# Optimization experiments

Hardware: AMD Instinct MI355X
Metric: run time of the kernel (lower is better)

Reference implementation:

```python
import jax, jax.numpy as jnp
import numpy as np

G = 160          # voxel grid extent per axis
N = 300000       # active voxels
CIN, COUT = 64, 128
EPS = 1e-4       # BatchNorm eps from module (0.0001)


def _neighbor_table(pos):
    """pos: [N,3] int32 in [0,G). Returns idx [27,N] int32, -1 where no neighbor voxel exists."""
    n = pos.shape[0]
    flat = (pos[:, 0] * G + pos[:, 1]) * G + pos[:, 2]
    grid = jnp.full((G * G * G,), -1, dtype=jnp.int32).at[flat].set(
        jnp.arange(n, dtype=jnp.int32))
    offs = jnp.array([[dx, dy, dz] for dx in (-1, 0, 1)
                      for dy in (-1, 0, 1) for dz in (-1, 0, 1)], dtype=jnp.int32)
    npos = pos[None, :, :] + offs[:, None, :]              # [27,N,3]
    inb = jnp.all((npos >= 0) & (npos < G), axis=-1)       # [27,N]
    nflat = (npos[..., 0] * G + npos[..., 1]) * G + npos[..., 2]
    nflat = jnp.where(inb, nflat, 0)
    return jnp.where(inb, grid[nflat], -1)                 # [27,N]


def _sparse_conv(feat, nbr_idx, W):
    """Submanifold sparse 3x3x3 conv. feat [N,Cin], nbr_idx [27,N], W [27,Cin,Cout]."""
    n = feat.shape[0]
    acc0 = jnp.zeros((n, W.shape[-1]), dtype=feat.dtype)

    def body(acc, xs):
        idx, Wk = xs                                       # [N], [Cin,Cout]
        valid = (idx >= 0)
        g = feat[jnp.maximum(idx, 0)] * valid[:, None].astype(feat.dtype)
        return acc + g @ Wk, None

    out, _ = jax.lax.scan(body, acc0, (nbr_idx, W))
    return out


def _bn(x, gamma, beta, mean, var):
    # eval-mode BatchNorm1d: (x - mean) / sqrt(var + eps) * gamma + beta
    return (x - mean) * jax.lax.rsqrt(var + EPS) * gamma + beta


def setup_inputs() -> dict:
    key = jax.random.key(0)
    ks = jax.random.split(key, 8)
    rng = np.random.default_rng(0)
    flat = rng.choice(G * G * G, size=N, replace=False)
    pos = np.stack(np.unravel_index(flat, (G, G, G)), axis=-1).astype(np.int32)

    feat = jax.random.normal(ks[0], (N, CIN), dtype=jnp.float32)
    lin_w = jax.random.normal(ks[1], (COUT, CIN), dtype=jnp.float32) / np.sqrt(CIN)
    W1 = jax.random.normal(ks[2], (27, CIN, COUT), dtype=jnp.float32) / np.sqrt(27 * CIN)
    W2 = jax.random.normal(ks[3], (27, COUT, COUT), dtype=jnp.float32) / np.sqrt(27 * COUT)
    return {
        "feat": feat,
        "pos": jnp.asarray(pos),
        "lin_w": lin_w,
        "bn1_gamma": jnp.ones((CIN,), jnp.float32),
        "bn1_beta": jnp.zeros((CIN,), jnp.float32),
        "bn1_mean": 0.1 * jax.random.normal(ks[4], (CIN,), dtype=jnp.float32),
        "bn1_var": 0.5 + jax.random.uniform(ks[5], (CIN,), dtype=jnp.float32),
        "W1": W1,
        "bn2_gamma": jnp.ones((COUT,), jnp.float32),
        "bn2_beta": jnp.zeros((COUT,), jnp.float32),
        "bn2_mean": 0.1 * jax.random.normal(ks[6], (COUT,), dtype=jnp.float32),
        "bn2_var": 0.5 + jax.random.uniform(ks[7], (COUT,), dtype=jnp.float32),
        "W2": W2,
    }


def reference(feat, pos, lin_w, bn1_gamma, bn1_beta, bn1_mean, bn1_var, W1,
              bn2_gamma, bn2_beta, bn2_mean, bn2_var, W2):
    nbr_idx = _neighbor_table(pos)                     # [27,N]
    out1 = feat @ lin_w.T                              # NetworkInNetwork skip
    h = jnp.maximum(_bn(feat, bn1_gamma, bn1_beta, bn1_mean, bn1_var), 0.0)  # LeakyReLU(0)==ReLU
    h = _sparse_conv(h, nbr_idx, W1)
    h = jnp.maximum(_bn(h, bn2_gamma, bn2_beta, bn2_mean, bn2_var), 0.0)
    h = _sparse_conv(h, nbr_idx, W2)
    return out1 + h
```

## Files before the change

kernel.cpp:

```cpp
#include <hip/hip_runtime.h>

#define G    160
#define G3   (G*G*G)
#define NV   300000
#define EPS  1e-4f
#define CAP  24576
#define CPAD 32
#define PCAP 655360
#define TOTIDX 896

typedef unsigned short u16;
typedef __attribute__((ext_vector_type(8))) short bf16x8;
typedef __attribute__((ext_vector_type(4))) float f32x4;

#define OFF_PART 0ull
#define OFF_GRID 0ull
#define OFF_PIN  167772160ull
#define OFF_PDST (OFF_PIN  + 2654208ull)
#define OFF_RI   (OFF_PDST + 2654208ull)
#define OFF_CNT  (OFF_RI   + 1200000ull)
#define OFF_H0   (OFF_CNT  + 4096ull)
#define OFF_H1   (OFF_H0   + 38400000ull)
#define OFF_W1T  (OFF_H1   + 76800000ull)
#define OFF_W2T  (OFF_W1T  + 442368ull)
#define OFF_LINW (OFF_W2T  + 884736ull)
#define OFF_BNP  (OFF_LINW + 16384ull)
#define WS_NEED  (OFF_BNP  + 1024ull)

__device__ __forceinline__ u16 f2bf(float f) {
  unsigned u = __float_as_uint(f);
  return (u16)((u + 0x7fffu + ((u >> 16) & 1u)) >> 16);
}
__device__ __forceinline__ float bf2f(u16 h) {
  return __uint_as_float(((unsigned)h) << 16);
}

__global__ void k_grid(const int* __restrict__ pos, int* __restrict__ grid) {
  int i = blockIdx.x * 256 + threadIdx.x;
  if (i < NV)
    grid[(pos[3*i] * G + pos[3*i+1]) * G + pos[3*i+2]] = i;
}

__global__ __launch_bounds__(256) void k_pairs(const int* __restrict__ pos,
                        const int* __restrict__ grid,
                        int* __restrict__ pin, int* __restrict__ pdst,
                        int* __restrict__ rowinfo, int* __restrict__ counts) {
  __shared__ int lcnt[27];
  __shared__ int wboff[27][4];
  __shared__ int gbase[27];
  __shared__ int scan[256];
  __shared__ int sgb;
  int t = threadIdx.x, lane = t & 63, wv = t >> 6;
  if (t < 27) lcnt[t] = 0;
  int i = blockIdx.x * 256 + t;
  bool act = (i < NV);
  int p0 = 0, p1 = 1 << 20, p2 = 0;
  if (act) { p0 = pos[3*i]; p1 = pos[3*i+1]; p2 = pos[3*i+2]; }
  __syncthreads();

  int j[26];
  #pragma unroll
  for (int kk = 0; kk < 26; kk++) {
    int k = kk < 13 ? kk : kk + 1;
    int q0 = p0 + k/9 - 1, q1 = p1 + (k/3)%3 - 1, q2 = p2 + k%3 - 1;
    bool inb = (q0 >= 0 && q0 < G && q1 >= 0 && q1 < G && q2 >= 0 && q2 < G);
    int addr = inb ? (q0*G + q1)*G + q2 : 0;
    int jj = grid[addr];
    j[kk] = inb ? jj : -1;
  }

  unsigned vmask = 0;
  #pragma unroll
  for (int kk = 0; kk < 26; kk++) if (j[kk] >= 0) vmask |= 1u << kk;
  int ci = __popc(vmask);

  unsigned long long m[26];
  #pragma unroll
  for (int kk = 0; kk < 26; kk++) m[kk] = __ballot(j[kk] >= 0);

  #pragma unroll
  for (int kk = 0; kk < 26; kk++) {
    int k = kk < 13 ? kk : kk + 1;
    if (lane == 0) wboff[k][wv] = atomicAdd(&lcnt[k], (int)__popcll(m[kk]));
  }
  scan[t] = ci;
  __syncthreads();
  #pragma unroll
  for (int d = 1; d < 256; d <<= 1) {
    int val = (t >= d) ? scan[t - d] : 0;
    __syncthreads();
    scan[t] += val;
    __syncthreads();
  }
  if (t < 27 && t != 13)
    gbase[t] = atomicAdd(&counts[t * CPAD], lcnt[t]);
  if (t == 255) sgb = atomicAdd(&counts[TOTIDX], scan[255]);
  __syncthreads();

  int rbase = sgb + scan[t] - ci;
  int cw = (rbase + ci > PCAP) ? 0 : ci;
  if (act) rowinfo[i] = (rbase << 5) | cw;

  #pragma unroll
  for (int kk = 0; kk < 26; kk++) {
    if (j[kk] >= 0) {
      int k = kk < 13 ? kk : kk + 1;
      int slot = gbase[k] + wboff[k][wv] + (int)__popcll(m[kk] & ((1ull << lane) - 1ull));
      int dst = rbase + __popc(vmask & ((1u << kk) - 1u));
      if (slot < CAP) {
        pin[k*CAP + slot]  = j[kk];
        pdst[k*CAP + slot] = (dst < PCAP) ? dst : -1;
      }
    }
  }
}

__global__ void k_bn1(const float* __restrict__ feat, const float* g, const float* b,
                      const float* m, const float* v, u16* __restrict__ h0) {
  __shared__ float ss[64], tt[64];
  int t = threadIdx.x;
  if (t < 64) { float s = g[t] * rsqrtf(v[t] + EPS); ss[t] = s; tt[t] = b[t] - m[t]*s; }
  __syncthreads();
  long gt = (long)blockIdx.x * 256 + t;
  if (gt >= (long)NV * 16) return;
  int c = (int)(gt & 15) * 4;
  float4 x = ((const float4*)feat)[gt];
  ushort4 q;
  q.x = f2bf(fmaxf(x.x*ss[c  ] + tt[c  ], 0.f));
  q.y = f2bf(fmaxf(x.y*ss[c+1] + tt[c+1], 0.f));
  q.z = f2bf(fmaxf(x.z*ss[c+2] + tt[c+2], 0.f));
  q.w = f2bf(fmaxf(x.w*ss[c+3] + tt[c+3], 0.f));
  ((ushort4*)h0)[gt] = q;
}

__global__ void k_weights(const float* __restrict__ W1, const float* __restrict__ W2,
                          const float* __restrict__ linw,
                          const float* __restrict__ g2, const float* __restrict__ b2,
                          const float* __restrict__ m2, const float* __restrict__ v2,
                          u16* __restrict__ w1t, u16* __restrict__ w2t, u16* __restrict__ lwt,
                          float* __restrict__ bnp) {
  __shared__ float tmp[8192];
  int b = blockIdx.x, t = threadIdx.x;
  if (b < 27) {
    const float* src = W1 + b * 8192;
    u16* dst = w1t + b * 8192;
    for (int u = t; u < 8192; u += 256) tmp[u] = src[u];
    __syncthreads();
    for (int u = t; u < 8192; u += 256) { int c = u >> 6, a = u & 63; dst[c*64 + a] = f2bf(tmp[a*128 + c]); }
  } else if (b < 54) {
    int k = b - 27;
    const float* src = W2 + k * 16384;
    u16* dst = w2t + k * 16384;
    for (int h = 0; h < 2; h++) {
      for (int u = t; u < 8192; u += 256) tmp[u] = src[h*8192 + u];
      __syncthreads();
      for (int u = t; u < 8192; u += 256) { int c = u >> 6, a = u & 63; dst[c*128 + h*64 + a] = f2bf(tmp[a*128 + c]); }
      __syncthreads();
    }
  } else if (b == 54) {
    for (int u = t; u < 8192; u += 256) lwt[u] = f2bf(linw[u]);
  } else {
    if (t < 128) { float s = g2[t] * rsqrtf(v2[t] + EPS); bnp[t] = s; bnp[128 + t] = b2[t] - m2[t]*s; }
  }
}

template<int K, int RS>
__device__ __forceinline__ void stage_rows(const u16* __restrict__ src, const int* sidx, u16* lds) {
  const int LPR = K / 8, RPI = 256 / LPR;
  int t = threadIdx.x, o = t % LPR, r0 = t / LPR;
  #pragma unroll
  for (int r = r0; r < 128; r += RPI) {
    int j = sidx[r];
    int4 val = make_int4(0, 0, 0, 0);
    if (j >= 0) val = *(const int4*)(src + (long)j * RS + o * 8);
    *(int4*)(lds + r * (K + 8) + o * 8) = val;
  }
}

__device__ __forceinline__ void stage_feat(const float* __restrict__ feat, int row0, u16* lds) {
  int t = threadIdx.x, o = t & 15, r0 = t >> 4;
  #pragma unroll
  for (int r = r0; r < 128; r += 16) {
    int row = row0 + r;
    float4 x = make_float4(0.f, 0.f, 0.f, 0.f);
    if (row < NV) x = *(const float4*)(feat + (long)row * 64 + o * 4);
    ushort4 q; q.x = f2bf(x.x); q.y = f2bf(x.y); q.z = f2bf(x.z); q.w = f2bf(x.w);
    *(ushort4*)(lds + r * 72 + o * 4) = q;
  }
}

template<int K>
__device__ __forceinline__ void mma_tile(const u16* As, const u16* __restrict__ wt, f32x4 acc[4][4]) {
  int lane = threadIdx.x & 63, wave = threadIdx.x >> 6;
  int wr = (wave >> 1) * 64, wc = (wave & 1) * 64;
  int lr = lane & 15, lk = (lane >> 4) * 8;
  #pragma unroll
  for (int kk = 0; kk < K; kk += 32) {
    bf16x8 a[4], b[4];
    #pragma unroll
    for (int f = 0; f < 4; f++) a[f] = *(const bf16x8*)(As + (wr + f*16 + lr) * (K + 8) + kk + lk);
    #pragma unroll
    for (int f = 0; f < 4; f++) b[f] = *(const bf16x8*)(wt + (wc + f*16 + lr) * K + kk + lk);
    #pragma unroll
    for (int fr = 0; fr < 4; fr++)
      #pragma unroll
      for (int fc = 0; fc < 4; fc++)
        acc[fr][fc] = __builtin_amdgcn_mfma_f32_16x16x32_bf16(a[fr], b[fc], acc[fr][fc], 0, 0, 0);
  }
}

__device__ __forceinline__ void spill_acc(const f32x4 acc[4][4], u16* As) {
  int t = threadIdx.x, lane = t & 63, wave = t >> 6;
  int wr = (wave >> 1) * 64, wc = (wave & 1) * 64, cr = (lane >> 4) * 4, cc = lane & 15;
  #pragma unroll
  for (int fr = 0; fr < 4; fr++)
    #pragma unroll
    for (int r = 0; r < 4; r++)
      #pragma unroll
      for (int fc = 0; fc < 4; fc++)
        As[(wr + fr*16 + cr + r) * 136 + wc + fc*16 + cc] = f2bf(acc[fr][fc][r]);
}

template<int K, int RS>
__global__ __launch_bounds__(256, 4) void k_scat(const u16* __restrict__ h, const u16* __restrict__ wt,
                                                 const int* __restrict__ pin,
                                                 const int* __restrict__ pdst,
                                                 const int* __restrict__ counts,
                                                 u16* __restrict__ partial) {
  int k = blockIdx.y;
  int cnt = counts[k * CPAD]; if (cnt > CAP) cnt = CAP;
  int base = blockIdx.x * 128;
  if (base >= cnt) return;
  __shared__ __align__(16) u16 As[128 * 136];
  __shared__ int sin[128], sdst[128];
  int t = threadIdx.x;
  if (t < 128) sin[t] = (base + t < cnt) ? pin[k*CAP + base + t] : -1;
  else         sdst[t - 128] = (base + t - 128 < cnt) ? pdst[k*CAP + base + t - 128] : -1;
  __syncthreads();
  stage_rows<K, RS>(h, sin, As);
  __syncthreads();
  f32x4 acc[4][4] = {};
  mma_tile<K>(As, wt + k * (K * 128), acc);
  __syncthreads();
  spill_acc(acc, As);
  __syncthreads();
  #pragma unroll
  for (int u = t; u < 2048; u += 256) {
    int r = u >> 4, o = u & 15;
    int d = sdst[r];
    if (d >= 0)
      *(int4*)(partial + (long)d * 128 + o * 8) = *(const int4*)(As + r * 136 + o * 8);
  }
}

__global__ __launch_bounds__(256, 4) void k_self1(const u16* __restrict__ h0,
                                                  const u16* __restrict__ w1t,
                                                  u16* __restrict__ h1) {
  __shared__ __align__(16) u16 As[128 * 136];
  __shared__ int sidx[128];
  int t = threadIdx.x, row0 = blockIdx.x * 128;
  if (t < 128) sidx[t] = (row0 + t < NV) ? row0 + t : -1;
  __syncthreads();
  stage_rows<64, 64>(h0, sidx, As);
  __syncthreads();
  f32x4 acc[4][4] = {};
  mma_tile<64>(As, w1t + 13 * 8192, acc);
  __syncthreads();
  spill_acc(acc, As);
  __syncthreads();
  #pragma unroll
  for (int u = t; u < 2048; u += 256) {
    int r = u >> 4, o = u & 15;
    if (row0 + r < NV)
      *(int4*)(h1 + (long)(row0 + r) * 128 + o * 8) = *(const int4*)(As + r * 136 + o * 8);
  }
}

__global__ __launch_bounds__(256, 4) void k_self2(const float* __restrict__ feat,
                                                  const u16* __restrict__ lwt,
                                                  u16* __restrict__ h1,
                                                  const u16* __restrict__ w2t) {
  __shared__ __align__(16) u16 As[128 * 136];
  __shared__ int sidx[128];
  int t = threadIdx.x, row0 = blockIdx.x * 128;
  if (t < 128) sidx[t] = (row0 + t < NV) ? row0 + t : -1;
  __syncthreads();
  f32x4 acc[4][4] = {};
  stage_feat(feat, row0, As);
  __syncthreads();
  mma_tile<64>(As, lwt, acc);
  __syncthreads();
  stage_rows<128, 128>(h1, sidx, As);
  __syncthreads();
  mma_tile<128>(As, w2t + 13 * 16384, acc);
  __syncthreads();
  spill_acc(acc, As);
  __syncthreads();
  #pragma unroll
  for (int u = t; u < 2048; u += 256) {
    int r = u >> 4, o = u & 15;
    if (row0 + r < NV)
      *(int4*)(h1 + (long)(row0 + r) * 128 + o * 8) = *(const int4*)(As + r * 136 + o * 8);
  }
}

__device__ __forceinline__ void gather_csr(int row, int q, int base, int cnt,
                                           const u16* __restrict__ sp,
                                           const u16* __restrict__ partial,
                                           float c[32]) {
  bf16x8 s0[4];
  const u16* srow = sp + (long)row * 128 + q * 32;
  #pragma unroll
  for (int u = 0; u < 4; u++) s0[u] = *(const bf16x8*)(srow + u * 8);
  #pragma unroll
  for (int u = 0; u < 4; u++)
    #pragma unroll
    for (int e = 0; e < 8; e++) c[u*8 + e] = bf2f((u16)s0[u][e]);
  const u16* pr = partial + (long)base * 128 + q * 32;
  int p = 0;
  for (; p + 2 <= cnt; p += 2) {
    bf16x8 a[4], b[4];
    #pragma unroll
    for (int u = 0; u < 4; u++) a[u] = *(const bf16x8*)(pr + u * 8);
    #pragma unroll
    for (int u = 0; u < 4; u++) b[u] = *(const bf16x8*)(pr + 128 + u * 8);
    #pragma unroll
    for (int u = 0; u < 4; u++)
      #pragma unroll
      for (int e = 0; e < 8; e++) c[u*8 + e] += bf2f((u16)a[u][e]) + bf2f((u16)b[u][e]);
    pr += 256;
  }
  if (p < cnt) {
    bf16x8 a[4];
    #pragma unroll
    for (int u = 0; u < 4; u++) a[u] = *(const bf16x8*)(pr + u * 8);
    #pragma unroll
    for (int u = 0; u < 4; u++)
      #pragma unroll
      for (int e = 0; e < 8; e++) c[u*8 + e] += bf2f((u16)a[u][e]);
  }
}

__global__ __launch_bounds__(256) void k_gather1(const int* __restrict__ rowinfo,
                                                 const u16* __restrict__ partial,
                                                 const float* __restrict__ bnp,
                                                 u16* __restrict__ h1) {
  long tid = (long)blockIdx.x * 256 + threadIdx.x;
  int row = (int)(tid >> 2), q = (int)(tid & 3);
  if (row >= NV) return;
  int ri = rowinfo[row];
  int base = (int)((unsigned)ri >> 5), cnt = ri & 31;
  float c[32];
  gather_csr(row, q, base, cnt, h1, partial, c);
  int col0 = q * 32;
  unsigned w[16];
  #pragma unroll
  for (int e = 0; e < 16; e++) {
    float o0 = fmaxf(c[2*e  ] * bnp[col0 + 2*e  ] + bnp[128 + col0 + 2*e  ], 0.f);
    float o1 = fmaxf(c[2*e+1] * bnp[col0 + 2*e+1] + bnp[128 + col0 + 2*e+1], 0.f);
    w[e] = (unsigned)f2bf(o0) | ((unsigned)f2bf(o1) << 16);
  }
  int4* dst = (int4*)(h1 + (long)row * 128 + col0);
  #pragma unroll
  for (int u = 0; u < 4; u++) dst[u] = make_int4(w[4*u], w[4*u+1], w[4*u+2], w[4*u+3]);
}

__global__ __launch_bounds__(256) void k_gather2(const int* __restrict__ rowinfo,
                                                 const u16* __restrict__ partial,
                                                 const u16* __restrict__ h1,
                                                 float* __restrict__ out) {
  long tid = (long)blockIdx.x * 256 + threadIdx.x;
  int row = (int)(tid >> 2), q = (int)(tid & 3);
  if (row >= NV) return;
  int ri = rowinfo[row];
  int base = (int)((unsigned)ri >> 5), cnt = ri & 31;
  float c[32];
  gather_csr(row, q, base, cnt, h1, partial, c);
  float* dst = out + (long)row * 128 + q * 32;
  #pragma unroll
  for (int u = 0; u < 8; u++) {
    f32x4 v;
    #pragma unroll
    for (int e = 0; e < 4; e++) v[e] = c[u*4 + e];
    *(f32x4*)(dst + u * 4) = v;
  }
}

extern "C" void kernel_launch(void* const* d_in, const int* in_sizes, int n_in,
                              void* d_out, int out_size, void* d_ws, size_t ws_size,
                              hipStream_t stream) {
  const float* feat = (const float*)d_in[0];
  const int*   pos  = (const int*)d_in[1];
  const float* linw = (const float*)d_in[2];
  const float* g1 = (const float*)d_in[3], *b1 = (const float*)d_in[4];
  const float* m1 = (const float*)d_in[5], *v1 = (const float*)d_in[6];
  const float* W1 = (const float*)d_in[7];
  const float* g2 = (const float*)d_in[8], *b2 = (const float*)d_in[9];
  const float* m2 = (const float*)d_in[10], *v2 = (const float*)d_in[11];
  const float* W2 = (const float*)d_in[12];

  if (ws_size < WS_NEED) return;

  char* ws = (char*)d_ws;
  u16*   partial = (u16*)(ws + OFF_PART);
  int*   grid    = (int*)(ws + OFF_GRID);
  int*   pin     = (int*)(ws + OFF_PIN);
  int*   pdst    = (int*)(ws + OFF_PDST);
  int*   rowinfo = (int*)(ws + OFF_RI);
  int*   counts  = (int*)(ws + OFF_CNT);
  u16*   h0      = (u16*)(ws + OFF_H0);
  u16*   h1      = (u16*)(ws + OFF_H1);
  u16*   w1t     = (u16*)(ws + OFF_W1T);
  u16*   w2t     = (u16*)(ws + OFF_W2T);
  u16*   lwt     = (u16*)(ws + OFF_LINW);
  float* bnp     = (float*)(ws + OFF_BNP);
  float* out     = (float*)d_out;

  hipMemsetAsync(grid,  0xFF, (size_t)G3 * 4, stream);
  hipMemsetAsync(counts, 0, 4096, stream);

  k_grid  <<<(NV + 255) / 256, 256, 0, stream>>>(pos, grid);
  k_pairs <<<(NV + 255) / 256, 256, 0, stream>>>(pos, grid, pin, pdst, rowinfo, counts);
  k_bn1   <<<(NV * 16) / 256, 256, 0, stream>>>(feat, g1, b1, m1, v1, h0);
  k_weights<<<56, 256, 0, stream>>>(W1, W2, linw, g2, b2, m2, v2, w1t, w2t, lwt, bnp);

  dim3 gt((NV + 127) / 128);
  dim3 gscat(CAP / 128, 27);
  dim3 gg(((long)NV * 4 + 255) / 256);
  k_scat<64, 64>   <<<gscat, 256, 0, stream>>>(h0, w1t, pin, pdst, counts, partial);
  k_self1          <<<gt, 256, 0, stream>>>(h0, w1t, h1);
  k_gather1        <<<gg, 256, 0, stream>>>(rowinfo, partial, bnp, h1);
  k_scat<128, 128> <<<gscat, 256, 0, stream>>>(h1, w2t, pin, pdst, counts, partial);
  k_self2          <<<gt, 256, 0, stream>>>(feat, lwt, h1, w2t);
  k_gather2        <<<gg, 256, 0, stream>>>(rowinfo, partial, h1, out);
}
```

Measured before the change: 676.8 us.

## Halve GEMM tile rows to 64 and fuse scatter with self conv1

Cuts the per-block row tile from 128 to 64 in the scatter and self-GEMM kernels. This halves the accumulator registers and LDS per block and raises the launch-bounds occupancy hint from 4 to 6. The first scatter and self kernels are merged into a single launch with a flat block index, which removes one launch and lets the two kinds of work overlap. The trade-off is twice as many blocks, with less weight reuse per block and more index and sync overhead.

```diff
diff --git a/kernel.cpp b/kernel.cpp
--- a/kernel.cpp
+++ b/kernel.cpp
@@ -8,6 +8,7 @@
 #define CPAD 32
 #define PCAP 655360
 #define TOTIDX 896
+#define NSCAT (27*384)
 
 typedef unsigned short u16;
 typedef __attribute__((ext_vector_type(8))) short bf16x8;
@@ -169,7 +170,7 @@
   const int LPR = K / 8, RPI = 256 / LPR;
   int t = threadIdx.x, o = t % LPR, r0 = t / LPR;
   #pragma unroll
-  for (int r = r0; r < 128; r += RPI) {
+  for (int r = r0; r < 64; r += RPI) {
     int j = sidx[r];
     int4 val = make_int4(0, 0, 0, 0);
     if (j >= 0) val = *(const int4*)(src + (long)j * RS + o * 8);
@@ -180,7 +181,7 @@
 __device__ __forceinline__ void stage_feat(const float* __restrict__ feat, int row0, u16* lds) {
   int t = threadIdx.x, o = t & 15, r0 = t >> 4;
   #pragma unroll
-  for (int r = r0; r < 128; r += 16) {
+  for (int r = r0; r < 64; r += 16) {
     int row = row0 + r;
     float4 x = make_float4(0.f, 0.f, 0.f, 0.f);
     if (row < NV) x = *(const float4*)(feat + (long)row * 64 + o * 4);
@@ -190,30 +191,30 @@
 }
 
 template<int K>
-__device__ __forceinline__ void mma_tile(const u16* As, const u16* __restrict__ wt, f32x4 acc[4][4]) {
+__device__ __forceinline__ void mma_tile(const u16* As, const u16* __restrict__ wt, f32x4 acc[2][4]) {
   int lane = threadIdx.x & 63, wave = threadIdx.x >> 6;
-  int wr = (wave >> 1) * 64, wc = (wave & 1) * 64;
+  int wr = (wave >> 1) * 32, wc = (wave & 1) * 64;
   int lr = lane & 15, lk = (lane >> 4) * 8;
   #pragma unroll
   for (int kk = 0; kk < K; kk += 32) {
-    bf16x8 a[4], b[4];
-    #pragma unroll
-    for (int f = 0; f < 4; f++) a[f] = *(const bf16x8*)(As + (wr + f*16 + lr) * (K + 8) + kk + lk);
+    bf16x8 a[2], b[4];
+    #pragma unroll
+    for (int f = 0; f < 2; f++) a[f] = *(const bf16x8*)(As + (wr + f*16 + lr) * (K + 8) + kk + lk);
     #pragma unroll
     for (int f = 0; f < 4; f++) b[f] = *(const bf16x8*)(wt + (wc + f*16 + lr) * K + kk + lk);
     #pragma unroll
-    for (int fr = 0; fr < 4; fr++)
+    for (int fr = 0; fr < 2; fr++)
       #pragma unroll
       for (int fc = 0; fc < 4; fc++)
         acc[fr][fc] = __builtin_amdgcn_mfma_f32_16x16x32_bf16(a[fr], b[fc], acc[fr][fc], 0, 0, 0);
   }
 }
 
-__device__ __forceinline__ void spill_acc(const f32x4 acc[4][4], u16* As) {
+__device__ __forceinline__ void spill_acc(const f32x4 acc[2][4], u16* As) {
   int t = threadIdx.x, lane = t & 63, wave = t >> 6;
-  int wr = (wave >> 1) * 64, wc = (wave & 1) * 64, cr = (lane >> 4) * 4, cc = lane & 15;
-  #pragma unroll
-  for (int fr = 0; fr < 4; fr++)
+  int wr = (wave >> 1) * 32, wc = (wave & 1) * 64, cr = (lane >> 4) * 4, cc = lane & 15;
+  #pragma unroll
+  for (int fr = 0; fr < 2; fr++)
     #pragma unroll
     for (int r = 0; r < 4; r++)
       #pragma unroll
@@ -221,31 +222,82 @@
         As[(wr + fr*16 + cr + r) * 136 + wc + fc*16 + cc] = f2bf(acc[fr][fc][r]);
 }
 
-template<int K, int RS>
-__global__ __launch_bounds__(256, 4) void k_scat(const u16* __restrict__ h, const u16* __restrict__ wt,
-                                                 const int* __restrict__ pin,
-                                                 const int* __restrict__ pdst,
-                                                 const int* __restrict__ counts,
-                                                 u16* __restrict__ partial) {
+__global__ __launch_bounds__(256, 6) void k_c1(const u16* __restrict__ h0,
+                                               const u16* __restrict__ w1t,
+                                               const int* __restrict__ pin,
+                                               const int* __restrict__ pdst,
+                                               const int* __restrict__ counts,
+                                               u16* __restrict__ partial,
+                                               u16* __restrict__ h1) {
+  __shared__ __align__(16) u16 As[64 * 136];
+  __shared__ int sin[64], sdst[64];
+  int bx = blockIdx.x, t = threadIdx.x;
+  if (bx < NSCAT) {
+    int k = bx / 384, base = (bx % 384) * 64;
+    int cnt = counts[k * CPAD]; if (cnt > CAP) cnt = CAP;
+    if (base >= cnt) return;
+    if (t < 64)       sin[t]       = (base + t < cnt)      ? pin[k*CAP + base + t]       : -1;
+    else if (t < 128) sdst[t - 64] = (base + t - 64 < cnt) ? pdst[k*CAP + base + t - 64] : -1;
+    __syncthreads();
+    stage_rows<64, 64>(h0, sin, As);
+    __syncthreads();
+    f32x4 acc[2][4] = {};
+    mma_tile<64>(As, w1t + k * 8192, acc);
+    __syncthreads();
+    spill_acc(acc, As);
+    __syncthreads();
+    #pragma unroll
+    for (int u = t; u < 1024; u += 256) {
+      int r = u >> 4, o = u & 15;
+      int d = sdst[r];
+      if (d >= 0)
+        *(int4*)(partial + (long)d * 128 + o * 8) = *(const int4*)(As + r * 136 + o * 8);
+    }
+  } else {
+    int row0 = (bx - NSCAT) * 64;
+    if (t < 64) sin[t] = (row0 + t < NV) ? row0 + t : -1;
+    __syncthreads();
+    stage_rows<64, 64>(h0, sin, As);
+    __syncthreads();
+    f32x4 acc[2][4] = {};
+    mma_tile<64>(As, w1t + 13 * 8192, acc);
+    __syncthreads();
+    spill_acc(acc, As);
+    __syncthreads();
+    #pragma unroll
+    for (int u = t; u < 1024; u += 256) {
+      int r = u >> 4, o = u & 15;
+      if (row0 + r < NV)
+        *(int4*)(h1 + (long)(row0 + r) * 128 + o * 8) = *(const int4*)(As + r * 136 + o * 8);
+    }
+  }
+}
+
+__global__ __launch_bounds__(256, 6) void k_scat2(const u16* __restrict__ h1,
+                                                  const u16* __restrict__ w2t,
+                                                  const int* __restrict__ pin,
+                                                  const int* __restrict__ pdst,
+                                                  const int* __restrict__ counts,
+                                                  u16* __restrict__ partial) {
   int k = blockIdx.y;
   int cnt = counts[k * CPAD]; if (cnt > CAP) cnt = CAP;
-  int base = blockIdx.x * 128;
+  int base = blockIdx.x * 64;
   if (base >= cnt) return;
-  __shared__ __align__(16) u16 As[128 * 136];
-  __shared__ int sin[128], sdst[128];
+  __shared__ __align__(16) u16 As[64 * 136];
+  __shared__ int sin[64], sdst[64];
   int t = threadIdx.x;
-  if (t < 128) sin[t] = (base + t < cnt) ? pin[k*CAP + base + t] : -1;
-  else         sdst[t - 128] = (base + t - 128 < cnt) ? pdst[k*CAP + base + t - 128] : -1;
-  __syncthreads();
-  stage_rows<K, RS>(h, sin, As);
-  __syncthreads();
-  f32x4 acc[4][4] = {};
-  mma_tile<K>(As, wt + k * (K * 128), acc);
+  if (t < 64)       sin[t]       = (base + t < cnt)      ? pin[k*CAP + base + t]       : -1;
+  else if (t < 128) sdst[t - 64] = (base + t - 64 < cnt) ? pdst[k*CAP + base + t - 64] : -1;
+  __syncthreads();
+  stage_rows<128, 128>(h1, sin, As);
+  __syncthreads();
+  f32x4 acc[2][4] = {};
+  mma_tile<128>(As, w2t + k * 16384, acc);
   __syncthreads();
   spill_acc(acc, As);
   __syncthreads();
   #pragma unroll
-  for (int u = t; u < 2048; u += 256) {
+  for (int u = t; u < 1024; u += 256) {
     int r = u >> 4, o = u & 15;
     int d = sdst[r];
     if (d >= 0)
@@ -253,39 +305,16 @@
   }
 }
 
-__global__ __launch_bounds__(256, 4) void k_self1(const u16* __restrict__ h0,
-                                                  const u16* __restrict__ w1t,
-                                                  u16* __restrict__ h1) {
-  __shared__ __align__(16) u16 As[128 * 136];
-  __shared__ int sidx[128];
-  int t = threadIdx.x, row0 = blockIdx.x * 128;
-  if (t < 128) sidx[t] = (row0 + t < NV) ? row0 + t : -1;
-  __syncthreads();
-  stage_rows<64, 64>(h0, sidx, As);
-  __syncthreads();
-  f32x4 acc[4][4] = {};
-  mma_tile<64>(As, w1t + 13 * 8192, acc);
-  __syncthreads();
-  spill_acc(acc, As);
-  __syncthreads();
-  #pragma unroll
-  for (int u = t; u < 2048; u += 256) {
-    int r = u >> 4, o = u & 15;
-    if (row0 + r < NV)
-      *(int4*)(h1 + (long)(row0 + r) * 128 + o * 8) = *(const int4*)(As + r * 136 + o * 8);
-  }
-}
-
-__global__ __launch_bounds__(256, 4) void k_self2(const float* __restrict__ feat,
+__global__ __launch_bounds__(256, 6) void k_self2(const float* __restrict__ feat,
                                                   const u16* __restrict__ lwt,
                                                   u16* __restrict__ h1,
                                                   const u16* __restrict__ w2t) {
-  __shared__ __align__(16) u16 As[128 * 136];
-  __shared__ int sidx[128];
-  int t = threadIdx.x, row0 = blockIdx.x * 128;
-  if (t < 128) sidx[t] = (row0 + t < NV) ? row0 + t : -1;
-  __syncthreads();
-  f32x4 acc[4][4] = {};
+  __shared__ __align__(16) u16 As[64 * 136];
+  __shared__ int sidx[64];
+  int t = threadIdx.x, row0 = blockIdx.x * 64;
+  if (t < 64) sidx[t] = (row0 + t < NV) ? row0 + t : -1;
+  __syncthreads();
+  f32x4 acc[2][4] = {};
   stage_feat(feat, row0, As);
   __syncthreads();
   mma_tile<64>(As, lwt, acc);
@@ -297,7 +326,7 @@
   spill_acc(acc, As);
   __syncthreads();
   #pragma unroll
-  for (int u = t; u < 2048; u += 256) {
+  for (int u = t; u < 1024; u += 256) {
     int r = u >> 4, o = u & 15;
     if (row0 + r < NV)
       *(int4*)(h1 + (long)(row0 + r) * 128 + o * 8) = *(const int4*)(As + r * 136 + o * 8);
@@ -424,13 +453,11 @@
   k_bn1   <<<(NV * 16) / 256, 256, 0, stream>>>(feat, g1, b1, m1, v1, h0);
   k_weights<<<56, 256, 0, stream>>>(W1, W2, linw, g2, b2, m2, v2, w1t, w2t, lwt, bnp);
 
-  dim3 gt((NV + 127) / 128);
-  dim3 gscat(CAP / 128, 27);
+  int nself = (NV + 63) / 64;
   dim3 gg(((long)NV * 4 + 255) / 256);
-  k_scat<64, 64>   <<<gscat, 256, 0, stream>>>(h0, w1t, pin, pdst, counts, partial);
-  k_self1          <<<gt, 256, 0, stream>>>(h0, w1t, h1);
-  k_gather1        <<<gg, 256, 0, stream>>>(rowinfo, partial, bnp, h1);
-  k_scat<128, 128> <<<gscat, 256, 0, stream>>>(h1, w2t, pin, pdst, counts, partial);
-  k_self2          <<<gt, 256, 0, stream>>>(feat, lwt, h1, w2t);
-  k_gather2        <<<gg, 256, 0, stream>>>(rowinfo, partial, h1, out);
-}
+  k_c1     <<<NSCAT + nself, 256, 0, stream>>>(h0, w1t, pin, pdst, counts, partial, h1);
+  k_gather1<<<gg, 256, 0, stream>>>(rowinfo, partial, bnp, h1);
+  k_scat2  <<<dim3(384, 27), 256, 0, stream>>>(h1, w2t, pin, pdst, counts, partial);
+  k_self2  <<<nself, 256, 0, stream>>>(feat, lwt, h1, w2t);
+  k_gather2<<<gg, 256, 0, stream>>>(rowinfo, partial, h1, out);
+}
```

After: 690.6 us. 2.0% more time.

## Merge prep kernels, fuse conv1 scatter with self-term, sort gather rows by neighbor count

Applied to the files above, without the earlier changes.

Folds the grid build, the BN1 pass and the weight transform into one prep launch, and merges the conv1 off-center scatter GEMM with the center self-term GEMM into a single launch. k_pairs now also builds a per-block permutation that groups rows by neighbor count, and both gather kernels walk rows in that order so adjacent threads loop over similar CSR lengths. The aim is fewer launches and less wave divergence in the gathers, at the cost of an extra perm array, one more indirection, and scattered output writes in the gathers.

```diff
diff --git a/kernel.cpp b/kernel.cpp
--- a/kernel.cpp
+++ b/kernel.cpp
@@ -8,6 +8,7 @@
 #define CPAD 32
 #define PCAP 655360
 #define TOTIDX 896
+#define NS1  (27*192)
 
 typedef unsigned short u16;
 typedef __attribute__((ext_vector_type(8))) short bf16x8;
@@ -18,8 +19,9 @@
 #define OFF_PIN  167772160ull
 #define OFF_PDST (OFF_PIN  + 2654208ull)
 #define OFF_RI   (OFF_PDST + 2654208ull)
-#define OFF_CNT  (OFF_RI   + 1200000ull)
-#define OFF_H0   (OFF_CNT  + 4096ull)
+#define OFF_PERM (OFF_RI   + 1200000ull)
+#define OFF_CNT  (OFF_PERM + 1200000ull)
+#define OFF_H0   (OFF_CNT  + 8192ull)
 #define OFF_H1   (OFF_H0   + 38400000ull)
 #define OFF_W1T  (OFF_H1   + 76800000ull)
 #define OFF_W2T  (OFF_W1T  + 442368ull)
@@ -35,23 +37,20 @@
   return __uint_as_float(((unsigned)h) << 16);
 }
 
-__global__ void k_grid(const int* __restrict__ pos, int* __restrict__ grid) {
-  int i = blockIdx.x * 256 + threadIdx.x;
-  if (i < NV)
-    grid[(pos[3*i] * G + pos[3*i+1]) * G + pos[3*i+2]] = i;
-}
-
 __global__ __launch_bounds__(256) void k_pairs(const int* __restrict__ pos,
                         const int* __restrict__ grid,
                         int* __restrict__ pin, int* __restrict__ pdst,
-                        int* __restrict__ rowinfo, int* __restrict__ counts) {
+                        int* __restrict__ rowinfo, int* __restrict__ perm,
+                        int* __restrict__ counts) {
   __shared__ int lcnt[27];
   __shared__ int wboff[27][4];
   __shared__ int gbase[27];
+  __shared__ int lclass[27];
+  __shared__ int coff[27];
   __shared__ int scan[256];
   __shared__ int sgb;
   int t = threadIdx.x, lane = t & 63, wv = t >> 6;
-  if (t < 27) lcnt[t] = 0;
+  if (t < 27) { lcnt[t] = 0; lclass[t] = 0; }
   int i = blockIdx.x * 256 + t;
   bool act = (i < NV);
   int p0 = 0, p1 = 1 << 20, p2 = 0;
@@ -74,6 +73,9 @@
   for (int kk = 0; kk < 26; kk++) if (j[kk] >= 0) vmask |= 1u << kk;
   int ci = __popc(vmask);
 
+  int myrank = 0;
+  if (act) myrank = atomicAdd(&lclass[ci], 1);
+
   unsigned long long m[26];
   #pragma unroll
   for (int kk = 0; kk < 26; kk++) m[kk] = __ballot(j[kk] >= 0);
@@ -95,11 +97,19 @@
   if (t < 27 && t != 13)
     gbase[t] = atomicAdd(&counts[t * CPAD], lcnt[t]);
   if (t == 255) sgb = atomicAdd(&counts[TOTIDX], scan[255]);
+  if (t == 0) {
+    int s = 0;
+    #pragma unroll
+    for (int c = 0; c < 27; c++) { coff[c] = s; s += lclass[c]; }
+  }
   __syncthreads();
 
   int rbase = sgb + scan[t] - ci;
   int cw = (rbase + ci > PCAP) ? 0 : ci;
-  if (act) rowinfo[i] = (rbase << 5) | cw;
+  if (act) {
+    rowinfo[i] = (rbase << 5) | cw;
+    perm[blockIdx.x * 256 + coff[ci] + myrank] = i;
+  }
 
   #pragma unroll
   for (int kk = 0; kk < 26; kk++) {
@@ -115,52 +125,62 @@
   }
 }
 
-__global__ void k_bn1(const float* __restrict__ feat, const float* g, const float* b,
-                      const float* m, const float* v, u16* __restrict__ h0) {
-  __shared__ float ss[64], tt[64];
-  int t = threadIdx.x;
-  if (t < 64) { float s = g[t] * rsqrtf(v[t] + EPS); ss[t] = s; tt[t] = b[t] - m[t]*s; }
-  __syncthreads();
-  long gt = (long)blockIdx.x * 256 + t;
-  if (gt >= (long)NV * 16) return;
-  int c = (int)(gt & 15) * 4;
-  float4 x = ((const float4*)feat)[gt];
-  ushort4 q;
-  q.x = f2bf(fmaxf(x.x*ss[c  ] + tt[c  ], 0.f));
-  q.y = f2bf(fmaxf(x.y*ss[c+1] + tt[c+1], 0.f));
-  q.z = f2bf(fmaxf(x.z*ss[c+2] + tt[c+2], 0.f));
-  q.w = f2bf(fmaxf(x.w*ss[c+3] + tt[c+3], 0.f));
-  ((ushort4*)h0)[gt] = q;
-}
-
-__global__ void k_weights(const float* __restrict__ W1, const float* __restrict__ W2,
+#define NB_BN   18750
+#define NB_GRID 1172
+__global__ __launch_bounds__(256) void k_prep(const float* __restrict__ feat,
+                          const int* __restrict__ pos, int* __restrict__ grid,
+                          const float* __restrict__ g1, const float* __restrict__ b1,
+                          const float* __restrict__ m1, const float* __restrict__ v1,
+                          u16* __restrict__ h0,
+                          const float* __restrict__ W1, const float* __restrict__ W2,
                           const float* __restrict__ linw,
                           const float* __restrict__ g2, const float* __restrict__ b2,
                           const float* __restrict__ m2, const float* __restrict__ v2,
-                          u16* __restrict__ w1t, u16* __restrict__ w2t, u16* __restrict__ lwt,
-                          float* __restrict__ bnp) {
-  __shared__ float tmp[8192];
+                          u16* __restrict__ w1t, u16* __restrict__ w2t,
+                          u16* __restrict__ lwt, float* __restrict__ bnp) {
+  __shared__ float shf[8192];
   int b = blockIdx.x, t = threadIdx.x;
-  if (b < 27) {
-    const float* src = W1 + b * 8192;
-    u16* dst = w1t + b * 8192;
-    for (int u = t; u < 8192; u += 256) tmp[u] = src[u];
-    __syncthreads();
-    for (int u = t; u < 8192; u += 256) { int c = u >> 6, a = u & 63; dst[c*64 + a] = f2bf(tmp[a*128 + c]); }
-  } else if (b < 54) {
-    int k = b - 27;
-    const float* src = W2 + k * 16384;
-    u16* dst = w2t + k * 16384;
-    for (int h = 0; h < 2; h++) {
-      for (int u = t; u < 8192; u += 256) tmp[u] = src[h*8192 + u];
+  if (b < NB_BN) {
+    float* ss = shf; float* tt = shf + 64;
+    if (t < 64) { float s = g1[t] * rsqrtf(v1[t] + EPS); ss[t] = s; tt[t] = b1[t] - m1[t]*s; }
+    __syncthreads();
+    long gt = (long)b * 256 + t;
+    int c = (int)(gt & 15) * 4;
+    float4 x = ((const float4*)feat)[gt];
+    ushort4 q;
+    q.x = f2bf(fmaxf(x.x*ss[c  ] + tt[c  ], 0.f));
+    q.y = f2bf(fmaxf(x.y*ss[c+1] + tt[c+1], 0.f));
+    q.z = f2bf(fmaxf(x.z*ss[c+2] + tt[c+2], 0.f));
+    q.w = f2bf(fmaxf(x.w*ss[c+3] + tt[c+3], 0.f));
+    ((ushort4*)h0)[gt] = q;
+  } else if (b < NB_BN + NB_GRID) {
+    int i = (b - NB_BN) * 256 + t;
+    if (i < NV)
+      grid[(pos[3*i] * G + pos[3*i+1]) * G + pos[3*i+2]] = i;
+  } else {
+    int bb = b - NB_BN - NB_GRID;
+    float* tmp = shf;
+    if (bb < 27) {
+      const float* src = W1 + bb * 8192;
+      u16* dst = w1t + bb * 8192;
+      for (int u = t; u < 8192; u += 256) tmp[u] = src[u];
       __syncthreads();
-      for (int u = t; u < 8192; u += 256) { int c = u >> 6, a = u & 63; dst[c*128 + h*64 + a] = f2bf(tmp[a*128 + c]); }
-      __syncthreads();
+      for (int u = t; u < 8192; u += 256) { int c = u >> 6, a = u & 63; dst[c*64 + a] = f2bf(tmp[a*128 + c]); }
+    } else if (bb < 54) {
+      int k = bb - 27;
+      const float* src = W2 + k * 16384;
+      u16* dst = w2t + k * 16384;
+      for (int h = 0; h < 2; h++) {
+        for (int u = t; u < 8192; u += 256) tmp[u] = src[h*8192 + u];
+        __syncthreads();
+        for (int u = t; u < 8192; u += 256) { int c = u >> 6, a = u & 63; dst[c*128 + h*64 + a] = f2bf(tmp[a*128 + c]); }
+        __syncthreads();
+      }
+    } else if (bb == 54) {
+      for (int u = t; u < 8192; u += 256) lwt[u] = f2bf(linw[u]);
+    } else {
+      if (t < 128) { float s = g2[t] * rsqrtf(v2[t] + EPS); bnp[t] = s; bnp[128 + t] = b2[t] - m2[t]*s; }
     }
-  } else if (b == 54) {
-    for (int u = t; u < 8192; u += 256) lwt[u] = f2bf(linw[u]);
-  } else {
-    if (t < 128) { float s = g2[t] * rsqrtf(v2[t] + EPS); bnp[t] = s; bnp[128 + t] = b2[t] - m2[t]*s; }
   }
 }
 
@@ -221,12 +241,63 @@
         As[(wr + fr*16 + cr + r) * 136 + wc + fc*16 + cc] = f2bf(acc[fr][fc][r]);
 }
 
-template<int K, int RS>
-__global__ __launch_bounds__(256, 4) void k_scat(const u16* __restrict__ h, const u16* __restrict__ wt,
-                                                 const int* __restrict__ pin,
-                                                 const int* __restrict__ pdst,
-                                                 const int* __restrict__ counts,
-                                                 u16* __restrict__ partial) {
+__global__ __launch_bounds__(256, 4) void k_c1(const u16* __restrict__ h0,
+                                               const u16* __restrict__ w1t,
+                                               const int* __restrict__ pin,
+                                               const int* __restrict__ pdst,
+                                               const int* __restrict__ counts,
+                                               u16* __restrict__ partial,
+                                               u16* __restrict__ h1) {
+  __shared__ __align__(16) u16 As[128 * 136];
+  __shared__ int sin[128], sdst[128];
+  int bx = blockIdx.x, t = threadIdx.x;
+  if (bx < NS1) {
+    int k = bx / 192, base = (bx % 192) * 128;
+    int cnt = counts[k * CPAD]; if (cnt > CAP) cnt = CAP;
+    if (base >= cnt) return;
+    if (t < 128) sin[t] = (base + t < cnt) ? pin[k*CAP + base + t] : -1;
+    else         sdst[t - 128] = (base + t - 128 < cnt) ? pdst[k*CAP + base + t - 128] : -1;
+    __syncthreads();
+    stage_rows<64, 64>(h0, sin, As);
+    __syncthreads();
+    f32x4 acc[4][4] = {};
+    mma_tile<64>(As, w1t + k * 8192, acc);
+    __syncthreads();
+    spill_acc(acc, As);
+    __syncthreads();
+    #pragma unroll
+    for (int u = t; u < 2048; u += 256) {
+      int r = u >> 4, o = u & 15;
+      int d = sdst[r];
+      if (d >= 0)
+        *(int4*)(partial + (long)d * 128 + o * 8) = *(const int4*)(As + r * 136 + o * 8);
+    }
+  } else {
+    int row0 = (bx - NS1) * 128;
+    if (t < 128) sin[t] = (row0 + t < NV) ? row0 + t : -1;
+    __syncthreads();
+    stage_rows<64, 64>(h0, sin, As);
+    __syncthreads();
+    f32x4 acc[4][4] = {};
+    mma_tile<64>(As, w1t + 13 * 8192, acc);
+    __syncthreads();
+    spill_acc(acc, As);
+    __syncthreads();
+    #pragma unroll
+    for (int u = t; u < 2048; u += 256) {
+      int r = u >> 4, o = u & 15;
+      if (row0 + r < NV)
+        *(int4*)(h1 + (long)(row0 + r) * 128 + o * 8) = *(const int4*)(As + r * 136 + o * 8);
+    }
+  }
+}
+
+__global__ __launch_bounds__(256, 4) void k_scat2(const u16* __restrict__ h1,
+                                                  const u16* __restrict__ w2t,
+                                                  const int* __restrict__ pin,
+                                                  const int* __restrict__ pdst,
+                                                  const int* __restrict__ counts,
+                                                  u16* __restrict__ partial) {
   int k = blockIdx.y;
   int cnt = counts[k * CPAD]; if (cnt > CAP) cnt = CAP;
   int base = blockIdx.x * 128;
@@ -237,10 +308,10 @@
   if (t < 128) sin[t] = (base + t < cnt) ? pin[k*CAP + base + t] : -1;
   else         sdst[t - 128] = (base + t - 128 < cnt) ? pdst[k*CAP + base + t - 128] : -1;
   __syncthreads();
-  stage_rows<K, RS>(h, sin, As);
+  stage_rows<128, 128>(h1, sin, As);
   __syncthreads();
   f32x4 acc[4][4] = {};
-  mma_tile<K>(As, wt + k * (K * 128), acc);
+  mma_tile<128>(As, w2t + k * 16384, acc);
   __syncthreads();
   spill_acc(acc, As);
   __syncthreads();
@@ -250,29 +321,6 @@
     int d = sdst[r];
     if (d >= 0)
       *(int4*)(partial + (long)d * 128 + o * 8) = *(const int4*)(As + r * 136 + o * 8);
-  }
-}
-
-__global__ __launch_bounds__(256, 4) void k_self1(const u16* __restrict__ h0,
-                                                  const u16* __restrict__ w1t,
-                                                  u16* __restrict__ h1) {
-  __shared__ __align__(16) u16 As[128 * 136];
-  __shared__ int sidx[128];
-  int t = threadIdx.x, row0 = blockIdx.x * 128;
-  if (t < 128) sidx[t] = (row0 + t < NV) ? row0 + t : -1;
-  __syncthreads();
-  stage_rows<64, 64>(h0, sidx, As);
-  __syncthreads();
-  f32x4 acc[4][4] = {};
-  mma_tile<64>(As, w1t + 13 * 8192, acc);
-  __syncthreads();
-  spill_acc(acc, As);
-  __syncthreads();
-  #pragma unroll
-  for (int u = t; u < 2048; u += 256) {
-    int r = u >> 4, o = u & 15;
-    if (row0 + r < NV)
-      *(int4*)(h1 + (long)(row0 + r) * 128 + o * 8) = *(const int4*)(As + r * 136 + o * 8);
   }
 }
 
@@ -341,13 +389,15 @@
   }
 }
 
-__global__ __launch_bounds__(256) void k_gather1(const int* __restrict__ rowinfo,
+__global__ __launch_bounds__(256) void k_gather1(const int* __restrict__ perm,
+                                                 const int* __restrict__ rowinfo,
                                                  const u16* __restrict__ partial,
                                                  const float* __restrict__ bnp,
                                                  u16* __restrict__ h1) {
   long tid = (long)blockIdx.x * 256 + threadIdx.x;
-  int row = (int)(tid >> 2), q = (int)(tid & 3);
-  if (row >= NV) return;
+  int idx = (int)(tid >> 2), q = (int)(tid & 3);
+  if (idx >= NV) return;
+  int row = perm[idx];
   int ri = rowinfo[row];
   int base = (int)((unsigned)ri >> 5), cnt = ri & 31;
   float c[32];
@@ -365,13 +415,15 @@
   for (int u = 0; u < 4; u++) dst[u] = make_int4(w[4*u], w[4*u+1], w[4*u+2], w[4*u+3]);
 }
 
-__global__ __launch_bounds__(256) void k_gather2(const int* __restrict__ rowinfo,
+__global__ __launch_bounds__(256) void k_gather2(const int* __restrict__ perm,
+                                                 const int* __restrict__ rowinfo,
                                                  const u16* __restrict__ partial,
                                                  const u16* __restrict__ h1,
                                                  float* __restrict__ out) {
   long tid = (long)blockIdx.x * 256 + threadIdx.x;
-  int row = (int)(tid >> 2), q = (int)(tid & 3);
-  if (row >= NV) return;
+  int idx = (int)(tid >> 2), q = (int)(tid & 3);
+  if (idx >= NV) return;
+  int row = perm[idx];
   int ri = rowinfo[row];
   int base = (int)((unsigned)ri >> 5), cnt = ri & 31;
   float c[32];
@@ -407,6 +459,7 @@
   int*   pin     = (int*)(ws + OFF_PIN);
   int*   pdst    = (int*)(ws + OFF_PDST);
   int*   rowinfo = (int*)(ws + OFF_RI);
+  int*   perm    = (int*)(ws + OFF_PERM);
   int*   counts  = (int*)(ws + OFF_CNT);
   u16*   h0      = (u16*)(ws + OFF_H0);
   u16*   h1      = (u16*)(ws + OFF_H1);
@@ -417,20 +470,18 @@
   float* out     = (float*)d_out;
 
   hipMemsetAsync(grid,  0xFF, (size_t)G3 * 4, stream);
-  hipMemsetAsync(counts, 0, 4096, stream);
-
-  k_grid  <<<(NV + 255) / 256, 256, 0, stream>>>(pos, grid);
-  k_pairs <<<(NV + 255) / 256, 256, 0, stream>>>(pos, grid, pin, pdst, rowinfo, counts);
-  k_bn1   <<<(NV * 16) / 256, 256, 0, stream>>>(feat, g1, b1, m1, v1, h0);
-  k_weights<<<56, 256, 0, stream>>>(W1, W2, linw, g2, b2, m2, v2, w1t, w2t, lwt, bnp);
-
-  dim3 gt((NV + 127) / 128);
-  dim3 gscat(CAP / 128, 27);
+  hipMemsetAsync(counts, 0, 8192, stream);
+
+  k_prep <<<NB_BN + NB_GRID + 56, 256, 0, stream>>>(feat, pos, grid, g1, b1, m1, v1, h0,
+                                                    W1, W2, linw, g2, b2, m2, v2,
+                                                    w1t, w2t, lwt, bnp);
+  k_pairs<<<(NV + 255) / 256, 256, 0, stream>>>(pos, grid, pin, pdst, rowinfo, perm, counts);
+
+  int nself = (NV + 127) / 128;
   dim3 gg(((long)NV * 4 + 255) / 256);
-  k_scat<64, 64>   <<<gscat, 256, 0, stream>>>(h0, w1t, pin, pdst, counts, partial);
-  k_self1          <<<gt, 256, 0, stream>>>(h0, w1t, h1);
-  k_gather1        <<<gg, 256, 0, stream>>>(rowinfo, partial, bnp, h1);
-  k_scat<128, 128> <<<gscat, 256, 0, stream>>>(h1, w2t, pin, pdst, counts, partial);
-  k_self2          <<<gt, 256, 0, stream>>>(feat, lwt, h1, w2t);
-  k_gather2        <<<gg, 256, 0, stream>>>(rowinfo, partial, h1, out);
-}
+  k_c1     <<<NS1 + nself, 256, 0, stream>>>(h0, w1t, pin, pdst, counts, partial, h1);
+  k_gather1<<<gg, 256, 0, stream>>>(perm, rowinfo, partial, bnp, h1);
+  k_scat2  <<<dim3(192, 27), 256, 0, stream>>>(h1, w2t, pin, pdst, counts, partial);
+  k_self2  <<<nself, 256, 0, stream>>>(feat, lwt, h1, w2t);
+  k_gather2<<<gg, 256, 0, stream>>>(perm, rowinfo, partial, h1, out);
+}
```

Result: slower. 702.7 us (+3.8%).
